# Performance work log

Measured on AMD Instinct MI355X. Metric: run time of the kernel, lower is better.

The kernel has to match this reference:

```python
import jax, jax.numpy as jnp
import numpy as np

SLOPE = 0.2  # LeakyReLU slope (DGCNN convention)

def _conv1x1(x, W, b):
    # x: [B, N, Cin], W: [Cout, Cin] -> [B, N, Cout] (Conv2d 1x1 == shared MLP)
    return jnp.einsum('bnc,oc->bno', x, W) + b

def _edgeconv(x, k, Wa, ba, Wb, bb):
    # DGCNN EdgeConv: kNN in feature space, edge MLP on (x_j - x_i, x_i), max-aggregate.
    # x: [B, N, C]
    sq = jnp.sum(x * x, axis=-1)                       # [B, N]
    inner = jnp.einsum('bnc,bmc->bnm', x, x)           # [B, N, N]
    dist = sq[:, :, None] - 2.0 * inner + sq[:, None, :]
    _, idx = jax.lax.top_k(-dist, k)                   # [B, N, k] (includes self)
    nb = jax.vmap(lambda xb, ib: xb[ib])(x, idx)       # [B, N, k, C] gather neighbors
    xi = jnp.broadcast_to(x[:, :, None, :], nb.shape)
    e = jnp.concatenate([nb - xi, xi], axis=-1)        # [B, N, k, 2C]
    h = jax.nn.leaky_relu(jnp.einsum('bnke,oe->bnko', e, Wa) + ba, SLOPE)
    h = jax.nn.leaky_relu(jnp.einsum('bnkc,oc->bnko', h, Wb) + bb, SLOPE)
    return jnp.max(h, axis=2)                          # [B, N, Cout]

def setup_inputs() -> dict:
    key = jax.random.key(0)
    ks = jax.random.split(key, 12)
    B, C, N = 2, 128, 8192
    r = 4
    out_dim = 3 * r  # 12
    def w(k, shape, fan_in):
        return (jax.random.normal(k, shape, jnp.float32) / np.sqrt(fan_in)).astype(jnp.float32)
    z = lambda n: jnp.zeros((n,), jnp.float32)
    return {
        'feature': jax.random.normal(ks[0], (B, C, N, 1), jnp.float32),
        # block 0: conv_bn_layer 128->32, EdgeConv(32->128, k=12)
        'Wc0': w(ks[1], (32, 128), 128), 'bc0': z(32),
        'We0a': w(ks[2], (128, 64), 64), 'be0a': z(128),
        'We0b': w(ks[3], (128, 128), 128), 'be0b': z(128),
        # block 1: conv_bn_layer 128->32, EdgeConv(32->128, k=4)
        'Wc1': w(ks[4], (32, 128), 128), 'bc1': z(32),
        'We1a': w(ks[5], (128, 64), 64), 'be1a': z(128),
        'We1b': w(ks[6], (128, 128), 128), 'be1b': z(128),
        # decoder: shared MLP [128 -> 6 -> 12], then Conv2d(12, 12, 1) with bias
        'Wd0': w(ks[7], (out_dim // 2, 128), 128), 'bd0': z(out_dim // 2),
        'Wd1': w(ks[8], (out_dim, out_dim // 2), out_dim // 2), 'bd1': z(out_dim),
        'Wd2': w(ks[9], (out_dim, out_dim), out_dim), 'bd2': z(out_dim),
    }

def reference(feature, Wc0, bc0, We0a, be0a, We0b, be0b,
              Wc1, bc1, We1a, be1a, We1b, be1b,
              Wd0, bd0, Wd1, bd1, Wd2, bd2):
    # feature: [B, C, N, 1] -> [B, N, C]
    x = jnp.swapaxes(jnp.squeeze(feature, -1), 1, 2)
    x = jax.nn.leaky_relu(_conv1x1(x, Wc0, bc0), SLOPE)   # 128 -> 32
    x = _edgeconv(x, 12, We0a, be0a, We0b, be0b)           # 32 -> 128, k=12
    x = jax.nn.leaky_relu(_conv1x1(x, Wc1, bc1), SLOPE)   # 128 -> 32
    x = _edgeconv(x, 4, We1a, be1a, We1b, be1b)            # 32 -> 128, k=4
    x = jax.nn.leaky_relu(_conv1x1(x, Wd0, bd0), SLOPE)   # 128 -> 6
    x = jax.nn.leaky_relu(_conv1x1(x, Wd1, bd1), SLOPE)   # 6 -> 12
    x = _conv1x1(x, Wd2, bd2)                              # final conv, no activation
    return x  # [B, N, 3*upsample_ratio] (matches squeeze(-1).permute(0,2,1))
```

## Files before the change

kernel.cpp:

```cpp
#include <hip/hip_runtime.h>

#define NPTS 8192
#define NB 2

typedef __attribute__((ext_vector_type(8))) short short8v;
typedef __attribute__((ext_vector_type(4))) float f32x4;

__device__ __forceinline__ float lrelu(float x) { return x > 0.f ? x : 0.2f * x; }
__device__ __forceinline__ float4 lrelu4(float4 a) {
    return make_float4(lrelu(a.x), lrelu(a.y), lrelu(a.z), lrelu(a.w));
}
__device__ __forceinline__ float4 fmax4(float4 a, float4 b) {
    return make_float4(fmaxf(a.x, b.x), fmaxf(a.y, b.y), fmaxf(a.z, b.z), fmaxf(a.w, b.w));
}
__device__ __forceinline__ float4 add4(float4 a, float4 b) {
    return make_float4(a.x + b.x, a.y + b.y, a.z + b.z, a.w + b.w);
}
__device__ __forceinline__ unsigned short f2bf(float f) {
    unsigned int u = __float_as_uint(f);
    return (unsigned short)((u + 0x7FFFu + ((u >> 16) & 1u)) >> 16);
}
__device__ __forceinline__ float bf2f(unsigned short h) {
    return __uint_as_float(((unsigned int)h) << 16);
}

__global__ void k_transpose_w(const float* __restrict__ Wb0, const float* __restrict__ Wb1,
                              float* __restrict__ out) {
    int t = blockIdx.x * 256 + threadIdx.x;
    if (t < 16384)      out[t] = Wb0[(t & 127) * 128 + (t >> 7)];
    else if (t < 32768) { int i = t - 16384; out[t] = Wb1[(i & 127) * 128 + (i >> 7)]; }
}

__device__ __forceinline__ void split3(float4 v, unsigned int* hp, unsigned int* mp,
                                       unsigned int* lp) {
    float c[4] = {v.x, v.y, v.z, v.w};
    unsigned short h[4], m[4], l[4];
    #pragma unroll
    for (int i = 0; i < 4; ++i) {
        h[i] = f2bf(c[i]);
        float r1 = c[i] - bf2f(h[i]);
        m[i] = f2bf(r1);
        float r2 = r1 - bf2f(m[i]);
        l[i] = f2bf(r2);
    }
    hp[0] = (unsigned int)h[0] | ((unsigned int)h[1] << 16);
    hp[1] = (unsigned int)h[2] | ((unsigned int)h[3] << 16);
    mp[0] = (unsigned int)m[0] | ((unsigned int)m[1] << 16);
    mp[1] = (unsigned int)m[2] | ((unsigned int)m[3] << 16);
    lp[0] = (unsigned int)l[0] | ((unsigned int)l[1] << 16);
    lp[1] = (unsigned int)l[2] | ((unsigned int)l[3] << 16);
}

__global__ void k_conv_in(const float* __restrict__ f, const float* __restrict__ W,
                          const float* __restrict__ bias, float* __restrict__ out,
                          float* __restrict__ sq, unsigned short* __restrict__ xh,
                          unsigned short* __restrict__ xm, unsigned short* __restrict__ xl) {
    int gid = blockIdx.x * blockDim.x + threadIdx.x;
    int b = gid >> 13, n = gid & (NPTS - 1);
    const float* fb = f + ((size_t)b << 20) + n;
    float acc[32];
    #pragma unroll
    for (int o = 0; o < 32; ++o) acc[o] = bias[o];
    #pragma unroll 4
    for (int c = 0; c < 128; ++c) {
        float xc = fb[(size_t)c * NPTS];
        #pragma unroll
        for (int o = 0; o < 32; ++o) acc[o] += xc * W[o * 128 + c];
    }
    float s = 0.f;
    float4* op = (float4*)(out + (size_t)gid * 32);
    unsigned int* hrow = (unsigned int*)(xh + (size_t)gid * 32);
    unsigned int* mrow = (unsigned int*)(xm + (size_t)gid * 32);
    unsigned int* lrow = (unsigned int*)(xl + (size_t)gid * 32);
    #pragma unroll
    for (int o4 = 0; o4 < 8; ++o4) {
        float4 v = make_float4(lrelu(acc[o4 * 4]), lrelu(acc[o4 * 4 + 1]),
                               lrelu(acc[o4 * 4 + 2]), lrelu(acc[o4 * 4 + 3]));
        s += v.x * v.x + v.y * v.y + v.z * v.z + v.w * v.w;
        op[o4] = v;
        unsigned int hp[2], mp[2], lp[2];
        split3(v, hp, mp, lp);
        *(uint2*)(hrow + o4 * 2) = make_uint2(hp[0], hp[1]);
        *(uint2*)(mrow + o4 * 2) = make_uint2(mp[0], mp[1]);
        *(uint2*)(lrow + o4 * 2) = make_uint2(lp[0], lp[1]);
    }
    sq[gid] = s;
}

__global__ __launch_bounds__(256, 2) void k_premix(const float* __restrict__ x,
                                                   const float* __restrict__ Wa,
                                                   const float* __restrict__ ba,
                                                   float* __restrict__ A,
                                                   float* __restrict__ Bm) {
    int tid = threadIdx.x;
    int q = tid >> 6;
    int p = blockIdx.x * 64 + (tid & 63);
    float4 xv[8];
    {
        const float4* xr = (const float4*)(x + (size_t)p * 32);
        #pragma unroll
        for (int u = 0; u < 8; ++u) xv[u] = xr[u];
    }
    const float* W0 = Wa + q * 32 * 64;
    float acc[32];
    #pragma unroll
    for (int o = 0; o < 32; ++o) acc[o] = 0.f;
    #pragma unroll 2
    for (int c4 = 0; c4 < 8; ++c4) {
        float4 v = xv[c4];
        #pragma unroll
        for (int o = 0; o < 32; ++o) {
            const float* w = W0 + o * 64 + c4 * 4;
            acc[o] += v.x * w[0] + v.y * w[1] + v.z * w[2] + v.w * w[3];
        }
    }
    {
        float4* op = (float4*)(A + (size_t)p * 128 + q * 32);
        #pragma unroll
        for (int o4 = 0; o4 < 8; ++o4)
            op[o4] = make_float4(acc[o4 * 4], acc[o4 * 4 + 1], acc[o4 * 4 + 2], acc[o4 * 4 + 3]);
    }
    #pragma unroll
    for (int o = 0; o < 32; ++o) acc[o] = ba[q * 32 + o];
    #pragma unroll 2
    for (int c4 = 0; c4 < 8; ++c4) {
        float4 v = xv[c4];
        #pragma unroll
        for (int o = 0; o < 32; ++o) {
            const float* w1 = W0 + o * 64 + c4 * 4;
            const float* w2 = w1 + 32;
            acc[o] += v.x * (w2[0] - w1[0]) + v.y * (w2[1] - w1[1]) +
                      v.z * (w2[2] - w1[2]) + v.w * (w2[3] - w1[3]);
        }
    }
    {
        float4* op = (float4*)(Bm + (size_t)p * 128 + q * 32);
        #pragma unroll
        for (int o4 = 0; o4 < 8; ++o4)
            op[o4] = make_float4(acc[o4 * 4], acc[o4 * 4 + 1], acc[o4 * 4 + 2], acc[o4 * 4 + 3]);
    }
}

template <int K, int JS, int C>
__global__ __launch_bounds__(128, 2) void k_knn_mfma(const unsigned short* __restrict__ xh,
                                                     const unsigned short* __restrict__ xm,
                                                     const unsigned short* __restrict__ xl,
                                                     const float* __restrict__ sqg,
                                                     float* __restrict__ cand_d,
                                                     int* __restrict__ cand_i) {
    constexpr int IT = 128;
    constexpr int JR = NPTS / JS;
    constexpr int NCH = JR / 16;
    constexpr int BPB = (NPTS / IT) * JS;
    constexpr int DS = 17;

    __shared__ float Dl[IT * DS];
    __shared__ float bufd[C * IT];
    __shared__ int   bufj[C * IT];

    int tid = threadIdx.x;
    int bid = blockIdx.x;
    int b = bid / BPB;
    int r0b = bid - b * BPB;
    int itile = r0b / JS;
    int jseg = r0b - itile * JS;

    const unsigned short* xhb = xh + ((size_t)b * NPTS) * 32;
    const unsigned short* xmb = xm + ((size_t)b * NPTS) * 32;
    const unsigned short* xlb = xl + ((size_t)b * NPTS) * 32;
    const float* sqb = sqg + (size_t)b * NPTS;

    int lane = tid & 63;
    int w = tid >> 6;
    int g = lane >> 4;
    int r15 = lane & 15;

    short8v ah[4], am[4], al[4];
    #pragma unroll
    for (int t = 0; t < 4; ++t) {
        size_t ii = (size_t)(itile * IT + w * 64 + t * 16 + r15);
        ah[t] = *(const short8v*)(xhb + ii * 32 + g * 8);
        am[t] = *(const short8v*)(xmb + ii * 32 + g * 8);
        al[t] = *(const short8v*)(xlb + ii * 32 + g * 8);
    }
    #pragma unroll
    for (int t = 0; t < 4; ++t) {
        asm volatile("" : "+v"(ah[t]));
        asm volatile("" : "+v"(am[t]));
        asm volatile("" : "+v"(al[t]));
    }

    float bd[K]; int bi[K];
    #pragma unroll
    for (int r = 0; r < K; ++r) { bd[r] = 1e30f; bi[r] = 0; }
    float thr = 1e30f;
    int cnt = 0;

    auto flush = [&]() {
        #pragma unroll
        for (int u = 0; u < C; ++u) {
            float dv = bufd[u * IT + tid];
            int jv = bufj[u * IT + tid];
            float dd = (u < cnt) ? dv : 1e30f;
            int ji = jv;
            #pragma unroll
            for (int r = 0; r < K; ++r) {
                bool c = dd < bd[r];
                float tf = bd[r]; int ti = bi[r];
                bd[r] = c ? dd : bd[r]; bi[r] = c ? ji : bi[r];
                dd = c ? tf : dd;       ji = c ? ti : ji;
            }
        }
        cnt = 0; thr = bd[K - 1];
    };

    int jbase = jseg * JR;
    #pragma unroll 1
    for (int ch = 0; ch < NCH; ++ch) {
        int j0 = jbase + ch * 16;
        short8v bh, bm, bl;
        {
            size_t ja = (size_t)(j0 + r15);
            bh = *(const short8v*)(xhb + ja * 32 + g * 8);
            bm = *(const short8v*)(xmb + ja * 32 + g * 8);
            bl = *(const short8v*)(xlb + ja * 32 + g * 8);
        }
        #pragma unroll
        for (int t = 0; t < 4; ++t) {
            f32x4 acc = {0.f, 0.f, 0.f, 0.f};
            acc = __builtin_amdgcn_mfma_f32_16x16x32_bf16(am[t], bm, acc, 0, 0, 0);
            acc = __builtin_amdgcn_mfma_f32_16x16x32_bf16(ah[t], bl, acc, 0, 0, 0);
            acc = __builtin_amdgcn_mfma_f32_16x16x32_bf16(al[t], bh, acc, 0, 0, 0);
            acc = __builtin_amdgcn_mfma_f32_16x16x32_bf16(ah[t], bm, acc, 0, 0, 0);
            acc = __builtin_amdgcn_mfma_f32_16x16x32_bf16(am[t], bh, acc, 0, 0, 0);
            acc = __builtin_amdgcn_mfma_f32_16x16x32_bf16(ah[t], bh, acc, 0, 0, 0);
            int il = w * 64 + t * 16 + g * 4;
            Dl[(il + 0) * DS + r15] = acc[0];
            Dl[(il + 1) * DS + r15] = acc[1];
            Dl[(il + 2) * DS + r15] = acc[2];
            Dl[(il + 3) * DS + r15] = acc[3];
        }
        #pragma unroll 1
        for (int jq = 0; jq < 16; jq += 4) {
            float v0 = Dl[tid * DS + jq + 0];
            float v1 = Dl[tid * DS + jq + 1];
            float v2 = Dl[tid * DS + jq + 2];
            float v3 = Dl[tid * DS + jq + 3];
            int j = j0 + jq;
            float d0 = sqb[j + 0] - 2.f * v0;
            float d1 = sqb[j + 1] - 2.f * v1;
            float d2 = sqb[j + 2] - 2.f * v2;
            float d3 = sqb[j + 3] - 2.f * v3;
            if (d0 < thr) { bufd[cnt * IT + tid] = d0; bufj[cnt * IT + tid] = j + 0; cnt++; }
            if (d1 < thr) { bufd[cnt * IT + tid] = d1; bufj[cnt * IT + tid] = j + 1; cnt++; }
            if (d2 < thr) { bufd[cnt * IT + tid] = d2; bufj[cnt * IT + tid] = j + 2; cnt++; }
            if (d3 < thr) { bufd[cnt * IT + tid] = d3; bufj[cnt * IT + tid] = j + 3; cnt++; }
            if (__any(cnt >= C - 3)) flush();
        }
    }
    flush();
    size_t base = ((size_t)jseg * (NB * NPTS) + (size_t)(b * NPTS) + itile * IT + tid) * K;
    #pragma unroll
    for (int r = 0; r < K; ++r) { cand_d[base + r] = bd[r]; cand_i[base + r] = bi[r]; }
}

template <int K, int JS>
__global__ __launch_bounds__(128, 4) void k_knn_merge2(const float* __restrict__ cand_d,
                                                       const int* __restrict__ cand_i,
                                                       int* __restrict__ idx_out) {
    int p = blockIdx.x * 128 + threadIdx.x;
    float bd[K]; int bi[K];
    #pragma unroll
    for (int r = 0; r < K; ++r) { bd[r] = 1e30f; bi[r] = 0; }
    float thr = 1e30f;
    #pragma unroll 1
    for (int s = 0; s < JS; ++s) {
        size_t base = ((size_t)s * (NB * NPTS) + p) * K;
        #pragma unroll 1
        for (int r = 0; r < K; ++r) {
            float d = cand_d[base + r];
            if (!(d < thr)) break;
            int j = cand_i[base + r];
            float dd = d; int ji = j;
            #pragma unroll
            for (int q = 0; q < K; ++q) {
                bool c = dd < bd[q];
                float tf = bd[q]; int ti = bi[q];
                bd[q] = c ? dd : bd[q]; bi[q] = c ? ji : bi[q];
                dd = c ? tf : dd;       ji = c ? ti : ji;
            }
            thr = bd[K - 1];
        }
    }
    int* op = idx_out + (size_t)p * K;
    #pragma unroll
    for (int r = 0; r < K; ++r) op[r] = bi[r];
}

template <int K>
__global__ __launch_bounds__(256, 1)
void k_edgeconv4(const int* __restrict__ idx,
                 const float* __restrict__ A, const float* __restrict__ Bm,
                 const float* __restrict__ WbTg, const float* __restrict__ bb,
                 float* __restrict__ y) {
    constexpr int TE = (K == 12) ? 6 : 4;
    constexpr int EPI = 16 * TE;
    constexpr int PI = EPI / K;
    constexpr int ITERS = 64 / PI;
    constexpr int NT = 256;
    constexpr int HS = 132;

    __shared__ __align__(16) float WbT[128 * 128];
    __shared__ __align__(16) float bb_s[128];
    __shared__ __align__(16) float H1[EPI * HS];
    __shared__ __align__(16) float Pm[(K == 12) ? 16 * 128 : 4];

    int tid = threadIdx.x;
    {
        const float4* sb = (const float4*)WbTg;
        float4* db = (float4*)WbT;
        #pragma unroll
        for (int i = 0; i < 16; ++i) db[tid + i * NT] = sb[tid + i * NT];
        if (tid < 128) bb_s[tid] = bb[tid];
    }

    int b = blockIdx.x >> 7;
    int pbase = (blockIdx.x & 127) * 64;
    const int* idxb = idx + ((size_t)b * NPTS) * K;
    const float4* A4 = (const float4*)(A + ((size_t)b * NPTS) * 128);
    const float4* B4 = (const float4*)(Bm + ((size_t)b * NPTS) * 128);
    float* yb = y + ((size_t)b * NPTS) * 128;

    int og = tid & 15;
    int eg = tid >> 4;
    int ebase = eg * TE;

    for (int it = 0; it < ITERS; ++it) {
        int pt0 = pbase + it * PI;
        #pragma unroll
        for (int r = 0; r < (EPI * 32) / NT; ++r) {
            int u = tid + r * NT;
            int e = u >> 5, c4 = u & 31;
            int p = pt0 + e / K;
            int j = idxb[(size_t)p * K + (e % K)];
            float4 av = A4[(size_t)j * 32 + c4];
            float4 bv = B4[(size_t)p * 32 + c4];
            *(float4*)&H1[e * HS + 4 * c4] = lrelu4(add4(av, bv));
        }
        __syncthreads();
        float4 acc[TE][2];
        {
            float4 blo = *(const float4*)&bb_s[og * 8];
            float4 bhi = *(const float4*)&bb_s[og * 8 + 4];
            #pragma unroll
            for (int e = 0; e < TE; ++e) { acc[e][0] = blo; acc[e][1] = bhi; }
        }
        #pragma unroll 2
        for (int c4 = 0; c4 < 32; ++c4) {
            float4 hv[TE];
            #pragma unroll
            for (int e = 0; e < TE; ++e)
                hv[e] = *(const float4*)&H1[(ebase + e) * HS + 4 * c4];
            #pragma unroll
            for (int j = 0; j < 4; ++j) {
                const float* wr = &WbT[(4 * c4 + j) * 128 + og * 8];
                float4 wlo = *(const float4*)wr;
                float4 whi = *(const float4*)(wr + 4);
                #pragma unroll
                for (int e = 0; e < TE; ++e) {
                    float hc = (j == 0) ? hv[e].x : (j == 1) ? hv[e].y : (j == 2) ? hv[e].z : hv[e].w;
                    acc[e][0].x += hc * wlo.x; acc[e][0].y += hc * wlo.y;
                    acc[e][0].z += hc * wlo.z; acc[e][0].w += hc * wlo.w;
                    acc[e][1].x += hc * whi.x; acc[e][1].y += hc * whi.y;
                    acc[e][1].z += hc * whi.z; acc[e][1].w += hc * whi.w;
                }
            }
        }
        float4 mlo = lrelu4(acc[0][0]), mhi = lrelu4(acc[0][1]);
        #pragma unroll
        for (int e = 1; e < TE; ++e) {
            mlo = fmax4(mlo, lrelu4(acc[e][0]));
            mhi = fmax4(mhi, lrelu4(acc[e][1]));
        }
        if constexpr (K == 4) {
            float4* yp = (float4*)&yb[((size_t)(pt0 + eg)) * 128 + og * 8];
            yp[0] = mlo; yp[1] = mhi;
            __syncthreads();
        } else {
            *(float4*)&Pm[eg * 128 + og * 8] = mlo;
            *(float4*)&Pm[eg * 128 + og * 8 + 4] = mhi;
            __syncthreads();
            #pragma unroll
            for (int r = 0; r < 4; ++r) {
                int u = tid + r * NT;
                int p = u >> 7, o = u & 127;
                yb[((size_t)(pt0 + p)) * 128 + o] =
                    fmaxf(Pm[(2 * p) * 128 + o], Pm[(2 * p + 1) * 128 + o]);
            }
        }
    }
}

__global__ void k_conv_mid(const float* __restrict__ xin, const float* __restrict__ W,
                           const float* __restrict__ bias, float* __restrict__ out,
                           float* __restrict__ sq, unsigned short* __restrict__ xh,
                           unsigned short* __restrict__ xm, unsigned short* __restrict__ xl) {
    int gid = blockIdx.x * blockDim.x + threadIdx.x;
    const float4* row = (const float4*)(xin + (size_t)gid * 128);
    float acc[32];
    #pragma unroll
    for (int o = 0; o < 32; ++o) acc[o] = bias[o];
    #pragma unroll 2
    for (int c4 = 0; c4 < 32; ++c4) {
        float4 v = row[c4];
        #pragma unroll
        for (int o = 0; o < 32; ++o) {
            const float* w = W + o * 128 + c4 * 4;
            acc[o] += v.x * w[0] + v.y * w[1] + v.z * w[2] + v.w * w[3];
        }
    }
    float s = 0.f;
    float4* op = (float4*)(out + (size_t)gid * 32);
    unsigned int* hrow = (unsigned int*)(xh + (size_t)gid * 32);
    unsigned int* mrow = (unsigned int*)(xm + (size_t)gid * 32);
    unsigned int* lrow = (unsigned int*)(xl + (size_t)gid * 32);
    #pragma unroll
    for (int o4 = 0; o4 < 8; ++o4) {
        float4 v = make_float4(lrelu(acc[o4 * 4]), lrelu(acc[o4 * 4 + 1]),
                               lrelu(acc[o4 * 4 + 2]), lrelu(acc[o4 * 4 + 3]));
        s += v.x * v.x + v.y * v.y + v.z * v.z + v.w * v.w;
        op[o4] = v;
        unsigned int hp[2], mp[2], lp[2];
        split3(v, hp, mp, lp);
        *(uint2*)(hrow + o4 * 2) = make_uint2(hp[0], hp[1]);
        *(uint2*)(mrow + o4 * 2) = make_uint2(mp[0], mp[1]);
        *(uint2*)(lrow + o4 * 2) = make_uint2(lp[0], lp[1]);
    }
    sq[gid] = s;
}

__global__ void k_decoder(const float* __restrict__ xin,
                          const float* __restrict__ W0, const float* __restrict__ b0,
                          const float* __restrict__ W1, const float* __restrict__ b1,
                          const float* __restrict__ W2, const float* __restrict__ b2,
                          float* __restrict__ out) {
    int gid = blockIdx.x * blockDim.x + threadIdx.x;
    const float4* row = (const float4*)(xin + (size_t)gid * 128);
    float h0[6];
    #pragma unroll
    for (int o = 0; o < 6; ++o) h0[o] = b0[o];
    #pragma unroll 4
    for (int c4 = 0; c4 < 32; ++c4) {
        float4 v = row[c4];
        #pragma unroll
        for (int o = 0; o < 6; ++o) {
            const float* w = W0 + o * 128 + c4 * 4;
            h0[o] += v.x * w[0] + v.y * w[1] + v.z * w[2] + v.w * w[3];
        }
    }
    #pragma unroll
    for (int o = 0; o < 6; ++o) h0[o] = lrelu(h0[o]);
    float h1[12];
    #pragma unroll
    for (int o = 0; o < 12; ++o) {
        float a = b1[o];
        #pragma unroll
        for (int j = 0; j < 6; ++j) a += W1[o * 6 + j] * h0[j];
        h1[o] = lrelu(a);
    }
    float* op = out + (size_t)gid * 12;
    #pragma unroll
    for (int o = 0; o < 12; ++o) {
        float a = b2[o];
        #pragma unroll
        for (int j = 0; j < 12; ++j) a += W2[o * 12 + j] * h1[j];
        op[o] = a;
    }
}

extern "C" void kernel_launch(void* const* d_in, const int* in_sizes, int n_in,
                              void* d_out, int out_size, void* d_ws, size_t ws_size,
                              hipStream_t stream) {
    const float* feature = (const float*)d_in[0];
    const float* Wc0 = (const float*)d_in[1];
    const float* bc0 = (const float*)d_in[2];
    const float* We0a = (const float*)d_in[3];
    const float* be0a = (const float*)d_in[4];
    const float* We0b = (const float*)d_in[5];
    const float* be0b = (const float*)d_in[6];
    const float* Wc1 = (const float*)d_in[7];
    const float* bc1 = (const float*)d_in[8];
    const float* We1a = (const float*)d_in[9];
    const float* be1a = (const float*)d_in[10];
    const float* We1b = (const float*)d_in[11];
    const float* be1b = (const float*)d_in[12];
    const float* Wd0 = (const float*)d_in[13];
    const float* bd0 = (const float*)d_in[14];
    const float* Wd1 = (const float*)d_in[15];
    const float* bd1 = (const float*)d_in[16];
    const float* Wd2 = (const float*)d_in[17];
    const float* bd2 = (const float*)d_in[18];
    float* out = (float*)d_out;

    float* f = (float*)d_ws;
    float* x0   = f;
    float* x1   = f + 524288;
    int*   idx0 = (int*)(f + 1048576);
    int*   idx1 = (int*)(f + 1245184);
    float* wT   = f + 1310720;
    float* Zab  = f + 1343488;
    float* Abuf = Zab;
    float* Bbuf = Zab + 2097152;
    float* Y    = f + 5537792;
    float* sq0  = f + 7634944;
    float* sq1  = f + 7651328;
    unsigned short* xh0 = (unsigned short*)(f + 524288);
    unsigned short* xm0 = (unsigned short*)(f + 786432);
    unsigned short* xl0 = (unsigned short*)(f + 1048576);
    float* c0d  = f + 1343488;
    int*   c0i  = (int*)(f + 4489216);
    unsigned short* xh1 = (unsigned short*)Zab;
    unsigned short* xm1 = (unsigned short*)(Zab + 262144);
    unsigned short* xl1 = (unsigned short*)(Zab + 524288);
    float* c1d  = Zab + 786432;
    int*   c1i  = (int*)(Zab + 1835008);
    float* WbT0 = wT;
    float* WbT1 = wT + 16384;

    k_transpose_w<<<128, 256, 0, stream>>>(We0b, We1b, wT);
    k_conv_in<<<64, 256, 0, stream>>>(feature, Wc0, bc0, x0, sq0, xh0, xm0, xl0);
    k_knn_mfma<12, 16, 10><<<2048, 128, 0, stream>>>(xh0, xm0, xl0, sq0, c0d, c0i);
    k_knn_merge2<12, 16><<<128, 128, 0, stream>>>(c0d, c0i, idx0);
    k_premix<<<256, 256, 0, stream>>>(x0, We0a, be0a, Abuf, Bbuf);
    k_edgeconv4<12><<<256, 256, 0, stream>>>(idx0, Abuf, Bbuf, WbT0, be0b, Y);
    k_conv_mid<<<64, 256, 0, stream>>>(Y, Wc1, bc1, x1, sq1, xh1, xm1, xl1);
    k_knn_mfma<4, 16, 8><<<2048, 128, 0, stream>>>(xh1, xm1, xl1, sq1, c1d, c1i);
    k_knn_merge2<4, 16><<<128, 128, 0, stream>>>(c1d, c1i, idx1);
    k_premix<<<256, 256, 0, stream>>>(x1, We1a, be1a, Abuf, Bbuf);
    k_edgeconv4<4><<<256, 256, 0, stream>>>(idx1, Abuf, Bbuf, WbT1, be1b, Y);
    k_decoder<<<64, 256, 0, stream>>>(Y, Wd0, bd0, Wd1, bd1, Wd2, bd2, out);
}
```

Before: 632.7 us.

## Double-buffer kNN neighbor operand loads and stage squared norms in LDS

Unrolls the kNN chunk loop by two and uses two register sets for the bf16 hi/mid/lo neighbor operands. The next chunk's global loads are issued before the current chunk's MFMAs and selection, so memory latency can overlap with compute. The per-j squared norms are staged into a small per-wave LDS array instead of being read from global inside the selection loop. This costs extra VGPRs, which may pressure occupancy under the launch bounds. It also assumes an even chunk count and relies on in-wave LDS ordering with no barrier.

Measured after the change: 634.1 us. No clear change (+0.2%).

```diff
diff --git a/kernel.cpp b/kernel.cpp
--- a/kernel.cpp
+++ b/kernel.cpp
@@ -155,6 +155,7 @@
     constexpr int DS = 17;
 
     __shared__ float Dl[IT * DS];
+    __shared__ float SQl[2][16];
     __shared__ float bufd[C * IT];
     __shared__ int   bufj[C * IT];
 
@@ -214,51 +215,85 @@
         cnt = 0; thr = bd[K - 1];
     };
 
+#define LOADB_(J, BH, BM, BL)                                                  \
+    do {                                                                       \
+        size_t ja_ = (size_t)(J) + r15;                                        \
+        BH = *(const short8v*)(xhb + ja_ * 32 + g * 8);                        \
+        BM = *(const short8v*)(xmb + ja_ * 32 + g * 8);                        \
+        BL = *(const short8v*)(xlb + ja_ * 32 + g * 8);                        \
+    } while (0)
+
+#define SQSTAGE_(J0)                                                           \
+    do {                                                                       \
+        if (g == 0) SQl[w][r15] = sqb[(J0) + r15];                             \
+    } while (0)
+
+#define MFMA_(BH, BM, BL)                                                      \
+    do {                                                                       \
+        _Pragma("unroll")                                                      \
+        for (int t = 0; t < 4; ++t) {                                          \
+            f32x4 acc = {0.f, 0.f, 0.f, 0.f};                                  \
+            acc = __builtin_amdgcn_mfma_f32_16x16x32_bf16(am[t], BM, acc, 0, 0, 0); \
+            acc = __builtin_amdgcn_mfma_f32_16x16x32_bf16(ah[t], BL, acc, 0, 0, 0); \
+            acc = __builtin_amdgcn_mfma_f32_16x16x32_bf16(al[t], BH, acc, 0, 0, 0); \
+            acc = __builtin_amdgcn_mfma_f32_16x16x32_bf16(ah[t], BM, acc, 0, 0, 0); \
+            acc = __builtin_amdgcn_mfma_f32_16x16x32_bf16(am[t], BH, acc, 0, 0, 0); \
+            acc = __builtin_amdgcn_mfma_f32_16x16x32_bf16(ah[t], BH, acc, 0, 0, 0); \
+            int il_ = w * 64 + t * 16 + g * 4;                                 \
+            Dl[(il_ + 0) * DS + r15] = acc[0];                                 \
+            Dl[(il_ + 1) * DS + r15] = acc[1];                                 \
+            Dl[(il_ + 2) * DS + r15] = acc[2];                                 \
+            Dl[(il_ + 3) * DS + r15] = acc[3];                                 \
+        }                                                                      \
+    } while (0)
+
+#define SELECT_(J0)                                                            \
+    do {                                                                       \
+        _Pragma("unroll 1")                                                    \
+        for (int jq = 0; jq < 16; jq += 4) {                                   \
+            float v0 = Dl[tid * DS + jq + 0];                                  \
+            float v1 = Dl[tid * DS + jq + 1];                                  \
+            float v2 = Dl[tid * DS + jq + 2];                                  \
+            float v3 = Dl[tid * DS + jq + 3];                                  \
+            float s0 = SQl[w][jq + 0];                                         \
+            float s1 = SQl[w][jq + 1];                                         \
+            float s2 = SQl[w][jq + 2];                                         \
+            float s3 = SQl[w][jq + 3];                                         \
+            int j_ = (J0) + jq;                                                \
+            float d0 = s0 - 2.f * v0;                                          \
+            float d1 = s1 - 2.f * v1;                                          \
+            float d2 = s2 - 2.f * v2;                                          \
+            float d3 = s3 - 2.f * v3;                                          \
+            if (d0 < thr) { bufd[cnt * IT + tid] = d0; bufj[cnt * IT + tid] = j_ + 0; cnt++; } \
+            if (d1 < thr) { bufd[cnt * IT + tid] = d1; bufj[cnt * IT + tid] = j_ + 1; cnt++; } \
+            if (d2 < thr) { bufd[cnt * IT + tid] = d2; bufj[cnt * IT + tid] = j_ + 2; cnt++; } \
+            if (d3 < thr) { bufd[cnt * IT + tid] = d3; bufj[cnt * IT + tid] = j_ + 3; cnt++; } \
+            if (__any(cnt >= C - 3)) flush();                                  \
+        }                                                                      \
+    } while (0)
+
     int jbase = jseg * JR;
+    short8v bhA, bmA, blA, bhB, bmB, blB;
+    LOADB_(jbase, bhA, bmA, blA);
     #pragma unroll 1
-    for (int ch = 0; ch < NCH; ++ch) {
+    for (int ch = 0; ch < NCH; ch += 2) {
         int j0 = jbase + ch * 16;
-        short8v bh, bm, bl;
-        {
-            size_t ja = (size_t)(j0 + r15);
-            bh = *(const short8v*)(xhb + ja * 32 + g * 8);
-            bm = *(const short8v*)(xmb + ja * 32 + g * 8);
-            bl = *(const short8v*)(xlb + ja * 32 + g * 8);
-        }
-        #pragma unroll
-        for (int t = 0; t < 4; ++t) {
-            f32x4 acc = {0.f, 0.f, 0.f, 0.f};
-            acc = __builtin_amdgcn_mfma_f32_16x16x32_bf16(am[t], bm, acc, 0, 0, 0);
-            acc = __builtin_amdgcn_mfma_f32_16x16x32_bf16(ah[t], bl, acc, 0, 0, 0);
-            acc = __builtin_amdgcn_mfma_f32_16x16x32_bf16(al[t], bh, acc, 0, 0, 0);
-            acc = __builtin_amdgcn_mfma_f32_16x16x32_bf16(ah[t], bm, acc, 0, 0, 0);
-            acc = __builtin_amdgcn_mfma_f32_16x16x32_bf16(am[t], bh, acc, 0, 0, 0);
-            acc = __builtin_amdgcn_mfma_f32_16x16x32_bf16(ah[t], bh, acc, 0, 0, 0);
-            int il = w * 64 + t * 16 + g * 4;
-            Dl[(il + 0) * DS + r15] = acc[0];
-            Dl[(il + 1) * DS + r15] = acc[1];
-            Dl[(il + 2) * DS + r15] = acc[2];
-            Dl[(il + 3) * DS + r15] = acc[3];
-        }
-        #pragma unroll 1
-        for (int jq = 0; jq < 16; jq += 4) {
-            float v0 = Dl[tid * DS + jq + 0];
-            float v1 = Dl[tid * DS + jq + 1];
-            float v2 = Dl[tid * DS + jq + 2];
-            float v3 = Dl[tid * DS + jq + 3];
-            int j = j0 + jq;
-            float d0 = sqb[j + 0] - 2.f * v0;
-            float d1 = sqb[j + 1] - 2.f * v1;
-            float d2 = sqb[j + 2] - 2.f * v2;
-            float d3 = sqb[j + 3] - 2.f * v3;
-            if (d0 < thr) { bufd[cnt * IT + tid] = d0; bufj[cnt * IT + tid] = j + 0; cnt++; }
-            if (d1 < thr) { bufd[cnt * IT + tid] = d1; bufj[cnt * IT + tid] = j + 1; cnt++; }
-            if (d2 < thr) { bufd[cnt * IT + tid] = d2; bufj[cnt * IT + tid] = j + 2; cnt++; }
-            if (d3 < thr) { bufd[cnt * IT + tid] = d3; bufj[cnt * IT + tid] = j + 3; cnt++; }
-            if (__any(cnt >= C - 3)) flush();
-        }
+        int j1 = j0 + 16;
+        SQSTAGE_(j0);
+        LOADB_(j1, bhB, bmB, blB);
+        MFMA_(bhA, bmA, blA);
+        SELECT_(j0);
+        SQSTAGE_(j1);
+        int j2 = (ch + 2 < NCH) ? j1 + 16 : jbase;
+        LOADB_(j2, bhA, bmA, blA);
+        MFMA_(bhB, bmB, blB);
+        SELECT_(j1);
     }
     flush();
+#undef LOADB_
+#undef SQSTAGE_
+#undef MFMA_
+#undef SELECT_
     size_t base = ((size_t)jseg * (NB * NPTS) + (size_t)(b * NPTS) + itile * IT + tid) * K;
     #pragma unroll
     for (int r = 0; r < K; ++r) { cand_d[base + r] = bd[r]; cand_i[base + r] = bi[r]; }
```
